# Optimization experiments

Measured on AMD Instinct MI355X. Metric: run time of the kernel, lower is better.

## Reference

```python
import jax, jax.numpy as jnp
import numpy as np

B, TN, TE = 64, 131072, 262144
QD, ND, ED, P = 768, 512, 512, 512


def setup_inputs() -> dict:
    key = jax.random.key(0)
    ks = jax.random.split(key, 20)
    s = 0.02  # weight init scale
    return {
        "question": jax.random.normal(ks[0], (B, QD), jnp.float32),
        "nodes": jax.random.normal(ks[1], (TN, ND), jnp.float32),
        "edges": jax.random.normal(ks[2], (TE, ED), jnp.float32),
        "W_nq": jax.random.normal(ks[3], (QD, P), jnp.float32) * s,
        "b_nq": jnp.zeros((P,), jnp.float32),
        "W_n": jax.random.normal(ks[4], (ND, P), jnp.float32) * s,
        "b_n": jnp.zeros((P,), jnp.float32),
        "w_nv": jax.random.normal(ks[5], (P,), jnp.float32) * s,
        "b_nv": jnp.zeros((), jnp.float32),
        "W_eq": jax.random.normal(ks[6], (QD, P), jnp.float32) * s,
        "b_eq": jnp.zeros((P,), jnp.float32),
        "W_e": jax.random.normal(ks[7], (ED, P), jnp.float32) * s,
        "b_e": jnp.zeros((P,), jnp.float32),
        "w_ev": jax.random.normal(ks[8], (P,), jnp.float32) * s,
        "b_ev": jnp.zeros((), jnp.float32),
        "node_gid": jnp.sort(jax.random.randint(ks[9], (TN,), 0, B, jnp.int32)),
        "edge_gid": jnp.sort(jax.random.randint(ks[10], (TE,), 0, B, jnp.int32)),
    }


def segment_softmax(scores, seg_ids, num_segments):
    # numerically stable softmax within each graph's segment
    m = jax.ops.segment_max(scores, seg_ids, num_segments=num_segments)
    e = jnp.exp(scores - m[seg_ids])
    z = jax.ops.segment_sum(e, seg_ids, num_segments=num_segments)
    return e / z[seg_ids]


def reference(question, nodes, edges, W_nq, b_nq, W_n, b_n, w_nv, b_nv,
              W_eq, b_eq, W_e, b_e, w_ev, b_ev, node_gid, edge_gid):
    # question-conditioned projections, broadcast to each graph's elements
    qn = question @ W_nq + b_nq                      # [B, P]
    qe = question @ W_eq + b_eq                      # [B, P]
    hn = nodes @ W_n + b_n                           # [TN, P]
    he = edges @ W_e + b_e                           # [TE, P]
    s_n = jnp.tanh(hn + qn[node_gid]) @ w_nv + b_nv  # [TN]
    s_e = jnp.tanh(he + qe[edge_gid]) @ w_ev + b_ev  # [TE]
    att_n = segment_softmax(s_n, node_gid, B)        # per-graph softmax over nodes
    att_e = segment_softmax(s_e, edge_gid, B)        # per-graph softmax over edges
    return att_n, att_e
```

## Files before the change

kernel.cpp:

```cpp
#include <hip/hip_runtime.h>
#include <hip/hip_bf16.h>


typedef __attribute__((ext_vector_type(4))) float  floatx4;
typedef __attribute__((ext_vector_type(8))) short  shortx8;

#define TN_CONST 131072
#define TE_CONST 262144

__device__ __forceinline__ unsigned short f2bf(float f) {
    union { float f; unsigned u; } v; v.f = f;
    unsigned u = v.u;
    unsigned r = (u + 0x7FFFu + ((u >> 16) & 1u)) >> 16;
    return (unsigned short)r;
}

__global__ void prep_wt_kernel(const float* __restrict__ Wn, const float* __restrict__ We,
                               unsigned short* __restrict__ Wtn, unsigned short* __restrict__ Wte)
{
    int c = blockIdx.x * 256 + threadIdx.x;
    const int sel = c >> 18;
    const int idx = c & 262143;
    const int p = idx >> 9, k = idx & 511;
    const float* W = sel ? We : Wn;
    unsigned short* Wt = sel ? Wte : Wtn;
    Wt[idx] = f2bf(W[(size_t)k * 512 + p]);
}

__global__ void prep_q_kernel(const float* __restrict__ question,
                              const float* __restrict__ Wnq, const float* __restrict__ bnq,
                              const float* __restrict__ bn,
                              const float* __restrict__ Weq, const float* __restrict__ beq,
                              const float* __restrict__ be,
                              float* __restrict__ Qpn, float* __restrict__ Qpe)
{
    const int b     = blockIdx.x;
    const int which = blockIdx.y;
    const int kc    = blockIdx.z;
    const int p     = threadIdx.x;
    const float* W  = which ? Weq : Wnq;
    const float* bq = which ? beq : bnq;
    const float* bh = which ? be  : bn;
    float* Qp       = which ? Qpe : Qpn;
    const float* q  = question + b * 768;
    float s = 0.f;
    const int kbeg = kc * 192, kend = kbeg + 192;
    for (int k = kbeg; k < kend; ++k) s += q[k] * W[(size_t)k * 512 + p];
    if (kc == 0) s += bq[p] + bh[p];
    atomicAdd(&Qp[b * 512 + p], s);
}

#define BM 32
#define BKK 32

__global__ __launch_bounds__(256, 3)
void fused_gemm_attn(const float* __restrict__ A,
                     const unsigned short* __restrict__ Bt,
                     const float* __restrict__ Qp,
                     const float* __restrict__ wv,
                     const float* __restrict__ bvp,
                     const int*   __restrict__ gid,
                     float* __restrict__ eout,
                     float* __restrict__ zglob)
{
    __shared__ unsigned short As[BM][BKK + 8];
    __shared__ unsigned short Bs[512][BKK + 8];
    __shared__ float sred[4][BM];
    __shared__ float zpart[64];

    const int tid  = threadIdx.x;
    const int wave = tid >> 6;
    const int lane = tid & 63;
    const int m16  = lane & 15;
    const int q4   = lane >> 4;
    const long r0  = (long)blockIdx.x * BM;

    floatx4 acc[2][8];
#pragma unroll
    for (int i = 0; i < 2; ++i)
#pragma unroll
        for (int j = 0; j < 8; ++j) acc[i][j] = (floatx4){0.f, 0.f, 0.f, 0.f};

    const int ar  = tid >> 3;
    const int akc = (tid & 7) << 2;
    const float* aptr = A + (size_t)(r0 + ar) * 512 + akc;

    for (int k0 = 0; k0 < 512; k0 += BKK) {
        __syncthreads();
        {
            const float4 v = *(const float4*)(aptr + k0);
            unsigned lo = ((unsigned)f2bf(v.y) << 16) | f2bf(v.x);
            unsigned hi = ((unsigned)f2bf(v.w) << 16) | f2bf(v.z);
            *(uint2*)&As[ar][akc] = make_uint2(lo, hi);
        }
#pragma unroll
        for (int i = 0; i < 8; ++i) {
            int c   = tid + i * 256;
            int br  = c >> 2;
            int bkc = (c & 3) << 3;
            uint4 v = *(const uint4*)(Bt + (size_t)br * 512 + k0 + bkc);
            *(uint4*)&Bs[br][bkc] = v;
        }
        __syncthreads();

        shortx8 af[2], bfr[8];
#pragma unroll
        for (int i = 0; i < 2; ++i)
            af[i] = *(const shortx8*)&As[i * 16 + m16][q4 * 8];
#pragma unroll
        for (int j = 0; j < 8; ++j)
            bfr[j] = *(const shortx8*)&Bs[wave * 128 + j * 16 + m16][q4 * 8];
#pragma unroll
        for (int i = 0; i < 2; ++i)
#pragma unroll
            for (int j = 0; j < 8; ++j)
                acc[i][j] = __builtin_amdgcn_mfma_f32_16x16x32_bf16(af[i], bfr[j], acc[i][j], 0, 0, 0);
    }

    const float bv = bvp[0];
#pragma unroll
    for (int i = 0; i < 2; ++i) {
#pragma unroll
        for (int reg = 0; reg < 4; ++reg) {
            const int row = i * 16 + q4 * 4 + reg;
            const int g   = gid[r0 + row];
            const float* qrow = Qp + (size_t)g * 512;
            float partial = 0.f;
#pragma unroll
            for (int j = 0; j < 8; ++j) {
                const int p = wave * 128 + j * 16 + m16;
                float h  = acc[i][j][reg] + qrow[p];
                float ex = __expf(2.f * h);
                float t  = (ex - 1.f) * __builtin_amdgcn_rcpf(ex + 1.f);
                partial += t * wv[p];
            }
            partial += __shfl_xor(partial, 1);
            partial += __shfl_xor(partial, 2);
            partial += __shfl_xor(partial, 4);
            partial += __shfl_xor(partial, 8);
            if (m16 == 0) sred[wave][row] = partial;
        }
    }
    if (tid < 64) zpart[tid] = 0.f;
    __syncthreads();
    if (tid < BM) {
        float s = sred[0][tid] + sred[1][tid] + sred[2][tid] + sred[3][tid] + bv;
        float e = __expf(s);
        eout[r0 + tid] = e;
        atomicAdd(&zpart[gid[r0 + tid]], e);
    }
    __syncthreads();
    if (tid < 64) {
        float v = zpart[tid];
        if (v != 0.f) atomicAdd(&zglob[tid], v);
    }
}

__global__ void norm_kernel(float* __restrict__ out, const int* __restrict__ ngid,
                            const int* __restrict__ egid, const float* __restrict__ z)
{
    int idx = blockIdx.x * 256 + threadIdx.x;
    float zz;
    if (idx < TN_CONST) zz = z[ngid[idx]];
    else                zz = z[64 + egid[idx - TN_CONST]];
    out[idx] = out[idx] / zz;
}

extern "C" void kernel_launch(void* const* d_in, const int* in_sizes, int n_in,
                              void* d_out, int out_size, void* d_ws, size_t ws_size,
                              hipStream_t stream)
{
    const float* question = (const float*)d_in[0];
    const float* nodes    = (const float*)d_in[1];
    const float* edges    = (const float*)d_in[2];
    const float* W_nq     = (const float*)d_in[3];
    const float* b_nq     = (const float*)d_in[4];
    const float* W_n      = (const float*)d_in[5];
    const float* b_n      = (const float*)d_in[6];
    const float* w_nv     = (const float*)d_in[7];
    const float* b_nv     = (const float*)d_in[8];
    const float* W_eq     = (const float*)d_in[9];
    const float* b_eq     = (const float*)d_in[10];
    const float* W_e      = (const float*)d_in[11];
    const float* b_e      = (const float*)d_in[12];
    const float* w_ev     = (const float*)d_in[13];
    const float* b_ev     = (const float*)d_in[14];
    const int* node_gid   = (const int*)d_in[15];
    const int* edge_gid   = (const int*)d_in[16];
    float* out = (float*)d_out;

    char* ws = (char*)d_ws;
    float*          z   = (float*)(ws);
    float*          Qpn = (float*)(ws + 512);
    float*          Qpe = (float*)(ws + 131584);
    unsigned short* Wtn = (unsigned short*)(ws + 262656);
    unsigned short* Wte = (unsigned short*)(ws + 786944);

    hipMemsetAsync(ws, 0, 262656, stream);

    prep_wt_kernel<<<2048, 256, 0, stream>>>(W_n, W_e, Wtn, Wte);
    prep_q_kernel<<<dim3(64, 2, 4), 512, 0, stream>>>(question, W_nq, b_nq, b_n,
                                                      W_eq, b_eq, b_e, Qpn, Qpe);
    fused_gemm_attn<<<TN_CONST / BM, 256, 0, stream>>>(nodes, Wtn, Qpn, w_nv, b_nv,
                                                       node_gid, out, z);
    fused_gemm_attn<<<TE_CONST / BM, 256, 0, stream>>>(edges, Wte, Qpe, w_ev, b_ev,
                                                       edge_gid, out + TN_CONST, z + 64);
    norm_kernel<<<1536, 256, 0, stream>>>(out, node_gid, edge_gid, z);
}
```

Measured before the change: 1.348 ms.

## Double the row tile to 64, use 8 waves, and prefetch next K-slab into registers

Each block now handles 64 rows with 512 threads, so each loaded B tile is reused across twice as many rows. The next A and B slabs are loaded into registers during the current step's MFMA work, overlapping global loads with compute. The transposed bf16 weights are stored pre-tiled by 32-wide K chunks so B-tile loads are contiguous. The epilogue caches group ids in shared memory and hoists the wv loads. In exchange the kernel adds an extra barrier per step and raises register pressure, with the launch bound changed to 512 threads and 2 blocks.

```diff
diff --git a/kernel.cpp b/kernel.cpp
--- a/kernel.cpp
+++ b/kernel.cpp
@@ -7,6 +7,9 @@
 
 #define TN_CONST 131072
 #define TE_CONST 262144
+#define BM 64
+#define BK 32
+#define NSTEP 16
 
 __device__ __forceinline__ unsigned short f2bf(float f) {
     union { float f; unsigned u; } v; v.f = f;
@@ -24,7 +27,7 @@
     const int p = idx >> 9, k = idx & 511;
     const float* W = sel ? We : Wn;
     unsigned short* Wt = sel ? Wte : Wtn;
-    Wt[idx] = f2bf(W[(size_t)k * 512 + p]);
+    Wt[((k >> 5) << 14) + (p << 5) + (k & 31)] = f2bf(W[(size_t)k * 512 + p]);
 }
 
 __global__ void prep_q_kernel(const float* __restrict__ question,
@@ -50,10 +53,7 @@
     atomicAdd(&Qp[b * 512 + p], s);
 }
 
-#define BM 32
-#define BKK 32
-
-__global__ __launch_bounds__(256, 3)
+__global__ __launch_bounds__(512, 2)
 void fused_gemm_attn(const float* __restrict__ A,
                      const unsigned short* __restrict__ Bt,
                      const float* __restrict__ Qp,
@@ -63,10 +63,11 @@
                      float* __restrict__ eout,
                      float* __restrict__ zglob)
 {
-    __shared__ unsigned short As[BM][BKK + 8];
-    __shared__ unsigned short Bs[512][BKK + 8];
-    __shared__ float sred[4][BM];
+    __shared__ unsigned short As[BM][BK + 8];
+    __shared__ unsigned short Bs[512][BK + 8];
+    __shared__ float sred[8][BM];
     __shared__ float zpart[64];
+    __shared__ int   gsh[64];
 
     const int tid  = threadIdx.x;
     const int wave = tid >> 6;
@@ -75,64 +76,97 @@
     const int q4   = lane >> 4;
     const long r0  = (long)blockIdx.x * BM;
 
-    floatx4 acc[2][8];
-#pragma unroll
-    for (int i = 0; i < 2; ++i)
-#pragma unroll
-        for (int j = 0; j < 8; ++j) acc[i][j] = (floatx4){0.f, 0.f, 0.f, 0.f};
+    floatx4 acc[4][4];
+#pragma unroll
+    for (int i = 0; i < 4; ++i)
+#pragma unroll
+        for (int j = 0; j < 4; ++j) acc[i][j] = (floatx4){0.f, 0.f, 0.f, 0.f};
 
     const int ar  = tid >> 3;
     const int akc = (tid & 7) << 2;
     const float* aptr = A + (size_t)(r0 + ar) * 512 + akc;
-
-    for (int k0 = 0; k0 < 512; k0 += BKK) {
+    const unsigned short* bptr = Bt + (size_t)tid * 8;
+
+    float4 apf[2];
+    uint4  bpf[4];
+
+    apf[0] = *(const float4*)(aptr);
+#pragma unroll
+    for (int i = 0; i < 4; ++i)
+        bpf[i] = *(const uint4*)(bptr + i * 4096);
+    apf[1] = *(const float4*)(aptr + BK);
+    {
+        const float4 v = apf[0];
+        unsigned lo = ((unsigned)f2bf(v.y) << 16) | f2bf(v.x);
+        unsigned hi = ((unsigned)f2bf(v.w) << 16) | f2bf(v.z);
+        *(uint2*)&As[ar][akc] = make_uint2(lo, hi);
+#pragma unroll
+        for (int i = 0; i < 4; ++i) {
+            const int c = tid + i * 512;
+            *(uint4*)&Bs[c >> 2][(c & 3) << 3] = bpf[i];
+        }
+    }
+
+#pragma unroll
+    for (int t = 0; t < NSTEP; ++t) {
         __syncthreads();
-        {
-            const float4 v = *(const float4*)(aptr + k0);
+        if (t + 1 < NSTEP) {
+#pragma unroll
+            for (int i = 0; i < 4; ++i)
+                bpf[i] = *(const uint4*)(bptr + (size_t)(t + 1) * 16384 + i * 4096);
+        }
+        if (t + 2 < NSTEP)
+            apf[t & 1] = *(const float4*)(aptr + (t + 2) * BK);
+
+        shortx8 af[4], bfr[4];
+#pragma unroll
+        for (int i = 0; i < 4; ++i)
+            af[i] = *(const shortx8*)&As[i * 16 + m16][q4 * 8];
+#pragma unroll
+        for (int j = 0; j < 4; ++j)
+            bfr[j] = *(const shortx8*)&Bs[wave * 64 + j * 16 + m16][q4 * 8];
+#pragma unroll
+        for (int i = 0; i < 4; ++i)
+#pragma unroll
+            for (int j = 0; j < 4; ++j)
+                acc[i][j] = __builtin_amdgcn_mfma_f32_16x16x32_bf16(af[i], bfr[j], acc[i][j], 0, 0, 0);
+
+        if (t + 1 < NSTEP) {
+            __syncthreads();
+            const float4 v = apf[(t + 1) & 1];
             unsigned lo = ((unsigned)f2bf(v.y) << 16) | f2bf(v.x);
             unsigned hi = ((unsigned)f2bf(v.w) << 16) | f2bf(v.z);
             *(uint2*)&As[ar][akc] = make_uint2(lo, hi);
-        }
-#pragma unroll
-        for (int i = 0; i < 8; ++i) {
-            int c   = tid + i * 256;
-            int br  = c >> 2;
-            int bkc = (c & 3) << 3;
-            uint4 v = *(const uint4*)(Bt + (size_t)br * 512 + k0 + bkc);
-            *(uint4*)&Bs[br][bkc] = v;
-        }
-        __syncthreads();
-
-        shortx8 af[2], bfr[8];
-#pragma unroll
-        for (int i = 0; i < 2; ++i)
-            af[i] = *(const shortx8*)&As[i * 16 + m16][q4 * 8];
-#pragma unroll
-        for (int j = 0; j < 8; ++j)
-            bfr[j] = *(const shortx8*)&Bs[wave * 128 + j * 16 + m16][q4 * 8];
-#pragma unroll
-        for (int i = 0; i < 2; ++i)
-#pragma unroll
-            for (int j = 0; j < 8; ++j)
-                acc[i][j] = __builtin_amdgcn_mfma_f32_16x16x32_bf16(af[i], bfr[j], acc[i][j], 0, 0, 0);
-    }
+#pragma unroll
+            for (int i = 0; i < 4; ++i) {
+                const int c = tid + i * 512;
+                *(uint4*)&Bs[c >> 2][(c & 3) << 3] = bpf[i];
+            }
+        }
+    }
+
+    if (tid < 64) { gsh[tid] = gid[r0 + tid]; zpart[tid] = 0.f; }
+    __syncthreads();
 
     const float bv = bvp[0];
-#pragma unroll
-    for (int i = 0; i < 2; ++i) {
+    float wvp[4];
+#pragma unroll
+    for (int j = 0; j < 4; ++j) wvp[j] = wv[wave * 64 + j * 16 + m16];
+
+#pragma unroll
+    for (int i = 0; i < 4; ++i) {
 #pragma unroll
         for (int reg = 0; reg < 4; ++reg) {
             const int row = i * 16 + q4 * 4 + reg;
-            const int g   = gid[r0 + row];
-            const float* qrow = Qp + (size_t)g * 512;
+            const int g   = gsh[row];
+            const float* qrow = Qp + (size_t)g * 512 + wave * 64 + m16;
             float partial = 0.f;
 #pragma unroll
-            for (int j = 0; j < 8; ++j) {
-                const int p = wave * 128 + j * 16 + m16;
-                float h  = acc[i][j][reg] + qrow[p];
+            for (int j = 0; j < 4; ++j) {
+                float h  = acc[i][j][reg] + qrow[j * 16];
                 float ex = __expf(2.f * h);
-                float t  = (ex - 1.f) * __builtin_amdgcn_rcpf(ex + 1.f);
-                partial += t * wv[p];
+                float tt = (ex - 1.f) * __builtin_amdgcn_rcpf(ex + 1.f);
+                partial += tt * wvp[j];
             }
             partial += __shfl_xor(partial, 1);
             partial += __shfl_xor(partial, 2);
@@ -141,13 +175,14 @@
             if (m16 == 0) sred[wave][row] = partial;
         }
     }
-    if (tid < 64) zpart[tid] = 0.f;
     __syncthreads();
     if (tid < BM) {
-        float s = sred[0][tid] + sred[1][tid] + sred[2][tid] + sred[3][tid] + bv;
+        float s = bv;
+#pragma unroll
+        for (int w = 0; w < 8; ++w) s += sred[w][tid];
         float e = __expf(s);
         eout[r0 + tid] = e;
-        atomicAdd(&zpart[gid[r0 + tid]], e);
+        atomicAdd(&zpart[gsh[tid]], e);
     }
     __syncthreads();
     if (tid < 64) {
@@ -201,9 +236,9 @@
     prep_wt_kernel<<<2048, 256, 0, stream>>>(W_n, W_e, Wtn, Wte);
     prep_q_kernel<<<dim3(64, 2, 4), 512, 0, stream>>>(question, W_nq, b_nq, b_n,
                                                       W_eq, b_eq, b_e, Qpn, Qpe);
-    fused_gemm_attn<<<TN_CONST / BM, 256, 0, stream>>>(nodes, Wtn, Qpn, w_nv, b_nv,
+    fused_gemm_attn<<<TN_CONST / BM, 512, 0, stream>>>(nodes, Wtn, Qpn, w_nv, b_nv,
                                                        node_gid, out, z);
-    fused_gemm_attn<<<TE_CONST / BM, 256, 0, stream>>>(edges, Wte, Qpe, w_ev, b_ev,
+    fused_gemm_attn<<<TE_CONST / BM, 512, 0, stream>>>(edges, Wte, Qpe, w_ev, b_ev,
                                                        edge_gid, out + TN_CONST, z + 64);
     norm_kernel<<<1536, 256, 0, stream>>>(out, node_gid, edge_gid, z);
 }
```

Result: slower. 1.796 ms (+33.2%).

## Pipeline GEMM with direct global-to-LDS loads, larger tile, and pre-tiled weights

Applied to the files above, without the earlier changes.

Restructures the fused GEMM-attention kernel to use global_load_lds async copies with a double-buffered B tile and a 4-deep A ring, synchronised by explicit vmcnt waits and barriers. The block grows to 512 threads and 64 rows, so each B tile is shared by two row-groups of waves. The weights are pre-tiled so B loads are contiguous. A is kept as fp32 in an XOR-swizzled LDS layout and converted to bf16 at fragment load time. This aims to hide memory latency and halve B tile traffic per row, at the cost of more LDS, occupancy limited to one block per CU, and fragile hand-counted waitcnts.

```diff
diff --git a/kernel.cpp b/kernel.cpp
--- a/kernel.cpp
+++ b/kernel.cpp
@@ -7,12 +7,21 @@
 
 #define TN_CONST 131072
 #define TE_CONST 262144
+#define BM 64
+#define BK 32
+#define NSTEP 16
 
 __device__ __forceinline__ unsigned short f2bf(float f) {
     union { float f; unsigned u; } v; v.f = f;
     unsigned u = v.u;
     unsigned r = (u + 0x7FFFu + ((u >> 16) & 1u)) >> 16;
     return (unsigned short)r;
+}
+
+__device__ __forceinline__ void gload16(const void* g, void* l) {
+    __builtin_amdgcn_global_load_lds((const __attribute__((address_space(1))) void*)g,
+                                     (__attribute__((address_space(3))) void*)l,
+                                     16, 0, 0);
 }
 
 __global__ void prep_wt_kernel(const float* __restrict__ Wn, const float* __restrict__ We,
@@ -24,7 +33,7 @@
     const int p = idx >> 9, k = idx & 511;
     const float* W = sel ? We : Wn;
     unsigned short* Wt = sel ? Wte : Wtn;
-    Wt[idx] = f2bf(W[(size_t)k * 512 + p]);
+    Wt[((k >> 5) << 14) + (p << 5) + (k & 31)] = f2bf(W[(size_t)k * 512 + p]);
 }
 
 __global__ void prep_q_kernel(const float* __restrict__ question,
@@ -50,10 +59,7 @@
     atomicAdd(&Qp[b * 512 + p], s);
 }
 
-#define BM 32
-#define BKK 32
-
-__global__ __launch_bounds__(256, 3)
+__global__ __launch_bounds__(512, 1)
 void fused_gemm_attn(const float* __restrict__ A,
                      const unsigned short* __restrict__ Bt,
                      const float* __restrict__ Qp,
@@ -63,91 +69,113 @@
                      float* __restrict__ eout,
                      float* __restrict__ zglob)
 {
-    __shared__ unsigned short As[BM][BKK + 8];
-    __shared__ unsigned short Bs[512][BKK + 8];
+    __shared__ float          As32[4][BM][BK];
+    __shared__ unsigned short Bs[2][512][BK];
     __shared__ float sred[4][BM];
     __shared__ float zpart[64];
+    __shared__ int   gsh[64];
 
     const int tid  = threadIdx.x;
     const int wave = tid >> 6;
     const int lane = tid & 63;
     const int m16  = lane & 15;
     const int q4   = lane >> 4;
+    const int wr   = wave >> 2;
+    const int wc   = wave & 3;
     const long r0  = (long)blockIdx.x * BM;
 
+    if (tid < 64) { gsh[tid] = gid[r0 + tid]; zpart[tid] = 0.f; }
+
+    const int arow = tid >> 3;
+    const int achk = tid & 7;
+    const float* asrc = A + (size_t)(r0 + arow) * 512 + ((achk ^ (arow & 7)) << 2);
+    const unsigned short* bsrc = Bt + (size_t)tid * 8;
+
     floatx4 acc[2][8];
 #pragma unroll
     for (int i = 0; i < 2; ++i)
 #pragma unroll
         for (int j = 0; j < 8; ++j) acc[i][j] = (floatx4){0.f, 0.f, 0.f, 0.f};
 
-    const int ar  = tid >> 3;
-    const int akc = (tid & 7) << 2;
-    const float* aptr = A + (size_t)(r0 + ar) * 512 + akc;
-
-    for (int k0 = 0; k0 < 512; k0 += BKK) {
-        __syncthreads();
-        {
-            const float4 v = *(const float4*)(aptr + k0);
-            unsigned lo = ((unsigned)f2bf(v.y) << 16) | f2bf(v.x);
-            unsigned hi = ((unsigned)f2bf(v.w) << 16) | f2bf(v.z);
-            *(uint2*)&As[ar][akc] = make_uint2(lo, hi);
-        }
-#pragma unroll
-        for (int i = 0; i < 8; ++i) {
-            int c   = tid + i * 256;
-            int br  = c >> 2;
-            int bkc = (c & 3) << 3;
-            uint4 v = *(const uint4*)(Bt + (size_t)br * 512 + k0 + bkc);
-            *(uint4*)&Bs[br][bkc] = v;
-        }
-        __syncthreads();
-
-        shortx8 af[2], bfr[8];
-#pragma unroll
-        for (int i = 0; i < 2; ++i)
-            af[i] = *(const shortx8*)&As[i * 16 + m16][q4 * 8];
-#pragma unroll
-        for (int j = 0; j < 8; ++j)
-            bfr[j] = *(const shortx8*)&Bs[wave * 128 + j * 16 + m16][q4 * 8];
-#pragma unroll
-        for (int i = 0; i < 2; ++i)
-#pragma unroll
-            for (int j = 0; j < 8; ++j)
-                acc[i][j] = __builtin_amdgcn_mfma_f32_16x16x32_bf16(af[i], bfr[j], acc[i][j], 0, 0, 0);
+#pragma unroll
+    for (int i = 0; i < 4; ++i)
+        gload16(bsrc + i * 4096, (char*)&Bs[0][0][0] + (tid + i * 512) * 16);
+    gload16(asrc,      (char*)&As32[0][0][0] + tid * 16);
+    gload16(asrc + 32, (char*)&As32[1][0][0] + tid * 16);
+
+#pragma unroll
+    for (int t = 0; t < NSTEP; ++t) {
+        if (t + 1 < NSTEP) {
+#pragma unroll
+            for (int i = 0; i < 4; ++i)
+                gload16(bsrc + (size_t)(t + 1) * 16384 + i * 4096,
+                        (char*)&Bs[(t + 1) & 1][0][0] + (tid + i * 512) * 16);
+        }
+        if (t + 2 < NSTEP)
+            gload16(asrc + (t + 2) * BK, (char*)&As32[(t + 2) & 3][0][0] + tid * 16);
+
+        if (t < NSTEP - 2)       asm volatile("s_waitcnt vmcnt(6)" ::: "memory");
+        else if (t == NSTEP - 2) asm volatile("s_waitcnt vmcnt(5)" ::: "memory");
+        else                     asm volatile("s_waitcnt vmcnt(0)" ::: "memory");
+        __builtin_amdgcn_s_barrier();
+
+        shortx8 af[2];
+#pragma unroll
+        for (int i = 0; i < 2; ++i) {
+            const int row = wr * 32 + i * 16 + m16;
+            const float* ap = &As32[t & 3][row][0];
+            const float4 lo = *(const float4*)(ap + (((q4 * 2 + 0) ^ (m16 & 7)) << 2));
+            const float4 hi = *(const float4*)(ap + (((q4 * 2 + 1) ^ (m16 & 7)) << 2));
+            shortx8 r;
+            r[0] = (short)f2bf(lo.x); r[1] = (short)f2bf(lo.y);
+            r[2] = (short)f2bf(lo.z); r[3] = (short)f2bf(lo.w);
+            r[4] = (short)f2bf(hi.x); r[5] = (short)f2bf(hi.y);
+            r[6] = (short)f2bf(hi.z); r[7] = (short)f2bf(hi.w);
+            af[i] = r;
+        }
+#pragma unroll
+        for (int j = 0; j < 8; ++j) {
+            const shortx8 bfr = *(const shortx8*)&Bs[t & 1][wc * 128 + j * 16 + m16][q4 * 8];
+#pragma unroll
+            for (int i = 0; i < 2; ++i)
+                acc[i][j] = __builtin_amdgcn_mfma_f32_16x16x32_bf16(af[i], bfr, acc[i][j], 0, 0, 0);
+        }
+        __builtin_amdgcn_s_barrier();
     }
 
     const float bv = bvp[0];
+    float wvp[8];
+#pragma unroll
+    for (int j = 0; j < 8; ++j) wvp[j] = wv[wc * 128 + j * 16 + m16];
+
 #pragma unroll
     for (int i = 0; i < 2; ++i) {
 #pragma unroll
         for (int reg = 0; reg < 4; ++reg) {
-            const int row = i * 16 + q4 * 4 + reg;
-            const int g   = gid[r0 + row];
-            const float* qrow = Qp + (size_t)g * 512;
+            const int row = wr * 32 + i * 16 + q4 * 4 + reg;
+            const int g   = gsh[row];
+            const float* qrow = Qp + (size_t)g * 512 + wc * 128 + m16;
             float partial = 0.f;
 #pragma unroll
             for (int j = 0; j < 8; ++j) {
-                const int p = wave * 128 + j * 16 + m16;
-                float h  = acc[i][j][reg] + qrow[p];
+                float h  = acc[i][j][reg] + qrow[j * 16];
                 float ex = __expf(2.f * h);
-                float t  = (ex - 1.f) * __builtin_amdgcn_rcpf(ex + 1.f);
-                partial += t * wv[p];
+                float tt = (ex - 1.f) * __builtin_amdgcn_rcpf(ex + 1.f);
+                partial += tt * wvp[j];
             }
             partial += __shfl_xor(partial, 1);
             partial += __shfl_xor(partial, 2);
             partial += __shfl_xor(partial, 4);
             partial += __shfl_xor(partial, 8);
-            if (m16 == 0) sred[wave][row] = partial;
-        }
-    }
-    if (tid < 64) zpart[tid] = 0.f;
+            if (m16 == 0) sred[wc][row] = partial;
+        }
+    }
     __syncthreads();
     if (tid < BM) {
-        float s = sred[0][tid] + sred[1][tid] + sred[2][tid] + sred[3][tid] + bv;
+        float s = bv + sred[0][tid] + sred[1][tid] + sred[2][tid] + sred[3][tid];
         float e = __expf(s);
         eout[r0 + tid] = e;
-        atomicAdd(&zpart[gid[r0 + tid]], e);
+        atomicAdd(&zpart[gsh[tid]], e);
     }
     __syncthreads();
     if (tid < 64) {
@@ -201,9 +229,9 @@
     prep_wt_kernel<<<2048, 256, 0, stream>>>(W_n, W_e, Wtn, Wte);
     prep_q_kernel<<<dim3(64, 2, 4), 512, 0, stream>>>(question, W_nq, b_nq, b_n,
                                                       W_eq, b_eq, b_e, Qpn, Qpe);
-    fused_gemm_attn<<<TN_CONST / BM, 256, 0, stream>>>(nodes, Wtn, Qpn, w_nv, b_nv,
+    fused_gemm_attn<<<TN_CONST / BM, 512, 0, stream>>>(nodes, Wtn, Qpn, w_nv, b_nv,
                                                        node_gid, out, z);
-    fused_gemm_attn<<<TE_CONST / BM, 256, 0, stream>>>(edges, Wte, Qpe, w_ev, b_ev,
+    fused_gemm_attn<<<TE_CONST / BM, 512, 0, stream>>>(edges, Wte, Qpe, w_ev, b_ev,
                                                        edge_gid, out + TN_CONST, z + 64);
     norm_kernel<<<1536, 256, 0, stream>>>(out, node_gid, edge_gid, z);
 }
```

Result: faster. 1.264 ms (-6.3%).
